# Optimization experiments

Measured on AMD Instinct MI355X. Metric: run time of the kernel, lower is better.

Reference implementation:

```python
import jax, jax.numpy as jnp
import numpy as np

E = 8        # number of sessions (experts)
N = 512      # per-session input width (max units)
P = 512      # n_channels (output width)
F = 100      # max_F time bins
B = 128      # batch of trials
SCALE = 1.0


def setup_inputs() -> dict:
    key = jax.random.key(0)
    kx, ke, k1, k2, k3, k4 = jax.random.split(key, 6)
    x = jax.random.normal(kx, (B, F, N), dtype=jnp.float32)
    eid = jax.random.randint(ke, (B,), 0, E, dtype=jnp.int32)
    # Per-session stitcher Linear(N, 2N) and projector Linear(2N, P), stacked.
    s1 = 1.0 / np.sqrt(N)
    s2 = 1.0 / np.sqrt(2 * N)
    W1 = jax.random.uniform(k1, (E, N, 2 * N), jnp.float32, -s1, s1)
    b1 = jax.random.uniform(k2, (E, 2 * N), jnp.float32, -s1, s1)
    W2 = jax.random.uniform(k3, (E, 2 * N, P), jnp.float32, -s2, s2)
    b2 = jax.random.uniform(k4, (E, P), jnp.float32, -s2, s2)
    return {"x": x, "eid": eid, "W1": W1, "b1": b1, "W2": W2, "b2": b2}


def reference(x, eid, W1, b1, W2, b2):
    # Grouped (per-session) Linear -> Softsign -> Linear, dispatched by eid.
    # Equivalent to the torch loop over unique eids with mask gather/scatter,
    # expressed as a gather of per-sample expert weights + batched matmul.
    w1 = W1[eid]                      # [B, N, 2N]
    stitched = jnp.einsum('bfn,bnh->bfh', x, w1) + b1[eid][:, None, :]
    act = stitched / (1.0 + jnp.abs(stitched))  # Softsign
    act = act * SCALE
    w2 = W2[eid]                      # [B, 2N, P]
    out = jnp.einsum('bfh,bhp->bfp', act, w2) + b2[eid][:, None, :]
    return out                        # [B, F, P]
```

## Files before the change

kernel.cpp:

```cpp
#include <hip/hip_runtime.h>
#include <hip/hip_bf16.h>

#define B_ 128
#define F_ 100
#define N_ 512
#define H_ 1024
#define P_ 512
#define E_ 8
#define BK 64
#define AROWS 112

typedef __attribute__((ext_vector_type(8))) short bf16x8;
typedef __attribute__((ext_vector_type(4))) float f32x4;

#define GLOAD16(g, l) __builtin_amdgcn_global_load_lds(                      \
    (const __attribute__((address_space(1))) void*)(g),                      \
    (__attribute__((address_space(3))) void*)(l), 16, 0, 0)

static __device__ __forceinline__ short f2bf(float f) {
    __hip_bfloat16 h = __float2bfloat16(f);
    short s;
    __builtin_memcpy(&s, &h, sizeof(s));
    return s;
}

__global__ __launch_bounds__(256) void prep(
    const float* __restrict__ x, const float* __restrict__ W1,
    const float* __restrict__ W2, const int* __restrict__ eid,
    short* __restrict__ xbf, short* __restrict__ W1T, short* __restrict__ W2T,
    int2* __restrict__ ttab) {
    __shared__ float tile[64][65];
    __shared__ int scnt[E_], sbase[E_];
    const int bx = blockIdx.x;
    const int t = threadIdx.x;
    if (bx < 3200) {
        const int g = bx * 256 + t;
        const int col = (g & 63) * 8;
        const int row = g >> 6;
        const float* xp = x + (size_t)row * N_ + col;
        const float4 v0 = *(const float4*)(xp);
        const float4 v1 = *(const float4*)(xp + 4);
        union { short s[8]; uint4 u; } o;
        o.s[0] = f2bf(v0.x); o.s[1] = f2bf(v0.y);
        o.s[2] = f2bf(v0.z); o.s[3] = f2bf(v0.w);
        o.s[4] = f2bf(v1.x); o.s[5] = f2bf(v1.y);
        o.s[6] = f2bf(v1.z); o.s[7] = f2bf(v1.w);
        *(uint4*)(xbf + (size_t)row * N_ + col) = o.u;
    } else if (bx < 5248) {
        const float* W; short* WT; int R, C, r0, c0, e;
        if (bx < 4224) {
            const int idx = bx - 3200;
            e = idx >> 7; const int i = idx & 127;
            W = W1; WT = W1T; R = N_; C = H_;
            r0 = (i >> 4) * 64; c0 = (i & 15) * 64;
        } else {
            const int idx = bx - 4224;
            e = idx >> 7; const int i = idx & 127;
            W = W2; WT = W2T; R = H_; C = P_;
            r0 = (i & 15) * 64; c0 = (i >> 4) * 64;
        }
        const float* Wp = W + (size_t)e * R * C;
        short* WTp = WT + (size_t)e * C * R;
        {
            const int c4 = (t & 15) * 4, r = t >> 4;
#pragma unroll
            for (int p = 0; p < 4; p++) {
                const int row = p * 16 + r;
                const float4 v = *(const float4*)(Wp + (size_t)(r0 + row) * C + c0 + c4);
                tile[row][c4 + 0] = v.x; tile[row][c4 + 1] = v.y;
                tile[row][c4 + 2] = v.z; tile[row][c4 + 3] = v.w;
            }
        }
        __syncthreads();
        {
            const int r8 = (t & 7) * 8, cl = t >> 3;
#pragma unroll
            for (int p = 0; p < 2; p++) {
                const int c = p * 32 + cl;
                union { short s[8]; uint4 u; } o;
#pragma unroll
                for (int j = 0; j < 8; j++) o.s[j] = f2bf(tile[r8 + j][c]);
                *(uint4*)(&WTp[(size_t)(c0 + c) * R + r0 + r8]) = o.u;
            }
        }
    } else {
        if (t < E_) scnt[t] = 0;
        __syncthreads();
        int my_e = 0;
        if (t < B_) { my_e = eid[t]; atomicAdd(&scnt[my_e], 1); }
        __syncthreads();
        if (t == 0) {
            int s = 0;
            for (int i = 0; i < E_; i++) { sbase[i] = s; s += scnt[i]; }
        }
        __syncthreads();
        if (t < B_) {
            const int pos = atomicAdd(&sbase[my_e], 1);
            ttab[pos] = make_int2(t, my_e);
        }
    }
}

template <int KDIM, int BN_, bool FIRST>
__global__ __launch_bounds__(256, 2) void gemm_kernel(
    const short* __restrict__ A,
    const short* __restrict__ WT,
    const float* __restrict__ bias,
    const int2* __restrict__ ttab,
    short* __restrict__ actout,
    float* __restrict__ out)
{
    constexpr int NCOLS = FIRST ? H_ : P_;
    constexpr int NI = BN_ / 32;
    constexpr int STAGE1 = (AROWS + BN_) * BK;
    constexpr int EPI_SH = 4 * 4096;
    constexpr int SBUF_SH = (2 * STAGE1 > EPI_SH) ? 2 * STAGE1 : EPI_SH;
    __shared__ short sbuf[SBUF_SH];
    const int slot = (blockIdx.x & 7) * 16 + (blockIdx.x >> 3);
    const int2 te = ttab[slot];
    const int trial = te.x, e = te.y;
    const int n0 = blockIdx.y * BN_;
    const int t = threadIdx.x;
    const int lane = t & 63, w = t >> 6;
    const int wm = (w >> 1) * 64, wn = (w & 1) * (BN_ / 2);
    const int l15 = lane & 15, quad = lane >> 4;
    const int lr = lane >> 3;
    const int lc = (((lane & 7) ^ lr) * 8);

    f32x4 acc[4][NI];
#pragma unroll
    for (int mi = 0; mi < 4; mi++)
#pragma unroll
        for (int ni = 0; ni < NI; ni++)
            acc[mi][ni] = (f32x4)(0.0f);

    float bv[NI];
#pragma unroll
    for (int ni = 0; ni < NI; ni++)
        bv[ni] = bias[(size_t)e * NCOLS + n0 + wn + ni * 16 + l15];

    const short* Ap = A + (size_t)trial * F_ * KDIM;
    const short* Bp = WT + ((size_t)e * NCOLS + n0) * KDIM;

    auto stage = [&](int k0, short* sb) {
        short* sA = sb;
        short* sB = sb + AROWS * BK;
#pragma unroll
        for (int i = 0; i < 4; i++) {
            const int rb = w * 32 + i * 8;
            if (rb < AROWS)
                GLOAD16(Ap + (size_t)(rb + lr) * KDIM + k0 + lc, &sA[rb * BK]);
        }
#pragma unroll
        for (int i = 0; i < NI; i++) {
            const int rb = w * (BN_ / 4) + i * 8;
            GLOAD16(Bp + (size_t)(rb + lr) * KDIM + k0 + lc, &sB[rb * BK]);
        }
    };

    auto compute = [&](const short* sb) {
        const short* sA = sb;
        const short* sB = sb + AROWS * BK;
#pragma unroll
        for (int ks = 0; ks < 2; ks++) {
            const int sw = (((ks * 4 + quad) ^ (l15 & 7)) * 8);
            bf16x8 af, bfr[NI];
#pragma unroll
            for (int ni = 0; ni < NI; ni++)
                bfr[ni] = *(const bf16x8*)(&sB[(wn + ni * 16 + l15) * BK + sw]);
#pragma unroll
            for (int mi = 0; mi < 4; mi++) {
                if (wm + mi * 16 < F_) {
                    af = *(const bf16x8*)(&sA[(wm + mi * 16 + l15) * BK + sw]);
#pragma unroll
                    for (int ni = 0; ni < NI; ni++)
                        acc[mi][ni] = __builtin_amdgcn_mfma_f32_16x16x32_bf16(af, bfr[ni], acc[mi][ni], 0, 0, 0);
                }
            }
        }
    };

    auto wait_prev_and_bar = [&]() {
        if (w < 3) asm volatile("s_waitcnt vmcnt(8)" ::: "memory");
        else       asm volatile("s_waitcnt vmcnt(6)" ::: "memory");
        __builtin_amdgcn_s_barrier();
        __builtin_amdgcn_sched_barrier(0);
    };
    auto bar = [&]() {
        __builtin_amdgcn_sched_barrier(0);
        __builtin_amdgcn_s_barrier();
        __builtin_amdgcn_sched_barrier(0);
    };

    short* b0 = sbuf;
    short* b1 = sbuf + STAGE1;

    stage(0, b0);
    for (int k0 = 0; k0 < KDIM - 2 * BK; k0 += 2 * BK) {
        stage(k0 + BK, b1);
        wait_prev_and_bar();
        compute(b0);
        bar();
        stage(k0 + 2 * BK, b0);
        wait_prev_and_bar();
        compute(b1);
        bar();
    }
    stage(KDIM - BK, b1);
    wait_prev_and_bar();
    compute(b0);
    bar();
    asm volatile("s_waitcnt vmcnt(0)" ::: "memory");
    __builtin_amdgcn_s_barrier();
    __builtin_amdgcn_sched_barrier(0);
    compute(b1);
    bar();

    if constexpr (FIRST) {
        short* sW = sbuf + w * 4096;
#pragma unroll
        for (int mi = 0; mi < 4; mi++) {
#pragma unroll
            for (int ni = 0; ni < 4; ni++) {
                const int cl = ni * 16 + l15;
#pragma unroll
                for (int r = 0; r < 4; r++) {
                    const int rl = mi * 16 + quad * 4 + r;
                    float v = acc[mi][ni][r] + bv[ni];
                    v = v / (1.0f + fabsf(v));
                    sW[rl * 64 + (((cl >> 3) ^ (rl & 7)) * 8) + (cl & 7)] = f2bf(v);
                }
            }
        }
#pragma unroll
        for (int i = 0; i < 8; i++) {
            const int rl = i * 8 + lr;
            const int c = lane & 7;
            const bf16x8 v = *(const bf16x8*)(&sW[rl * 64 + ((c ^ lr) * 8)]);
            const int grow = wm + rl;
            if (grow < F_)
                *(bf16x8*)(&actout[((size_t)trial * F_ + grow) * H_ + n0 + wn + c * 8]) = v;
        }
    } else {
        float* fW = (float*)(sbuf) + w * 2048;
#pragma unroll
        for (int pass = 0; pass < NI; pass += 2) {
#pragma unroll
            for (int mi = 0; mi < 4; mi++) {
#pragma unroll
                for (int nj = 0; nj < 2; nj++) {
                    const int cl = nj * 16 + l15;
#pragma unroll
                    for (int r = 0; r < 4; r++) {
                        const int rl = mi * 16 + quad * 4 + r;
                        fW[rl * 32 + (((cl >> 2) ^ (rl & 7)) * 4) + (cl & 3)] =
                            acc[mi][pass + nj][r] + bv[pass + nj];
                    }
                }
            }
#pragma unroll
            for (int i = 0; i < 8; i++) {
                const int rl = i * 8 + lr;
                const int c = lane & 7;
                const float4 v = *(const float4*)(&fW[rl * 32 + ((c ^ lr) * 4)]);
                const int grow = wm + rl;
                if (grow < F_)
                    *(float4*)(&out[((size_t)trial * F_ + grow) * P_ + n0 + wn + pass * 16 + c * 4]) = v;
            }
        }
    }
}

extern "C" void kernel_launch(void* const* d_in, const int* in_sizes, int n_in,
                              void* d_out, int out_size, void* d_ws, size_t ws_size,
                              hipStream_t stream) {
    const float* x  = (const float*)d_in[0];
    const int* eid  = (const int*)d_in[1];
    const float* W1 = (const float*)d_in[2];
    const float* b1 = (const float*)d_in[3];
    const float* W2 = (const float*)d_in[4];
    const float* b2 = (const float*)d_in[5];
    float* out = (float*)d_out;

    char* ws = (char*)d_ws;
    short* W1T = (short*)(ws);
    short* W2T = (short*)(ws + (size_t)(8u << 20));
    short* act = (short*)(ws + (size_t)(16u << 20));
    short* xbf = (short*)(ws + (size_t)(43u << 20));
    int2* ttab = (int2*)(ws + (size_t)(57u << 20));

    prep<<<dim3(5249), 256, 0, stream>>>(x, W1, W2, eid, xbf, W1T, W2T, ttab);
    gemm_kernel<N_, 128, true><<<dim3(B_, H_ / 128), 256, 0, stream>>>(xbf, W1T, b1, ttab, act, nullptr);
    gemm_kernel<H_, 128, false><<<dim3(B_, P_ / 128), 256, 0, stream>>>(act, W2T, b2, ttab, nullptr, out);
}
```

Baseline: 151.2 us.

## Load weight fragments directly into registers, stage only activations in LDS

The B (weight) operand is no longer staged through shared memory. Each wave now loads its MFMA B fragments straight from global memory into registers, double-buffered across k-steps, while the A tiles stay in LDS via global_load_lds. This halves LDS use per block, so launch bounds go from 2 to 3 blocks per CU, and it removes the LDS reads for B. The cost is more VGPR pressure and uncoalesced 16-byte global loads per lane. The vmcnt wait counts were retuned for the new load mix, which risks ordering bugs if the counts are wrong.

```diff
diff --git a/kernel.cpp b/kernel.cpp
--- a/kernel.cpp
+++ b/kernel.cpp
@@ -101,8 +101,8 @@
     }
 }
 
-template <int KDIM, int BN_, bool FIRST>
-__global__ __launch_bounds__(256, 2) void gemm_kernel(
+template <int KDIM, bool FIRST>
+__global__ __launch_bounds__(256, 3) void gemm_kernel(
     const short* __restrict__ A,
     const short* __restrict__ WT,
     const float* __restrict__ bias,
@@ -111,18 +111,18 @@
     float* __restrict__ out)
 {
     constexpr int NCOLS = FIRST ? H_ : P_;
-    constexpr int NI = BN_ / 32;
-    constexpr int STAGE1 = (AROWS + BN_) * BK;
+    constexpr int NI = 4;
+    constexpr int ASTAGE = AROWS * BK;
     constexpr int EPI_SH = 4 * 4096;
-    constexpr int SBUF_SH = (2 * STAGE1 > EPI_SH) ? 2 * STAGE1 : EPI_SH;
+    constexpr int SBUF_SH = (2 * ASTAGE > EPI_SH) ? 2 * ASTAGE : EPI_SH;
     __shared__ short sbuf[SBUF_SH];
     const int slot = (blockIdx.x & 7) * 16 + (blockIdx.x >> 3);
     const int2 te = ttab[slot];
     const int trial = te.x, e = te.y;
-    const int n0 = blockIdx.y * BN_;
+    const int n0 = blockIdx.y * 128;
     const int t = threadIdx.x;
     const int lane = t & 63, w = t >> 6;
-    const int wm = (w >> 1) * 64, wn = (w & 1) * (BN_ / 2);
+    const int wm = (w >> 1) * 64, wn = (w & 1) * 64;
     const int l15 = lane & 15, quad = lane >> 4;
     const int lr = lane >> 3;
     const int lc = (((lane & 7) ^ lr) * 8);
@@ -140,49 +140,47 @@
         bv[ni] = bias[(size_t)e * NCOLS + n0 + wn + ni * 16 + l15];
 
     const short* Ap = A + (size_t)trial * F_ * KDIM;
-    const short* Bp = WT + ((size_t)e * NCOLS + n0) * KDIM;
-
-    auto stage = [&](int k0, short* sb) {
-        short* sA = sb;
-        short* sB = sb + AROWS * BK;
+    const short* Bp = WT + ((size_t)e * NCOLS + n0 + wn + l15) * KDIM;
+
+    auto stage = [&](int k0, short* sA) {
 #pragma unroll
         for (int i = 0; i < 4; i++) {
             const int rb = w * 32 + i * 8;
             if (rb < AROWS)
                 GLOAD16(Ap + (size_t)(rb + lr) * KDIM + k0 + lc, &sA[rb * BK]);
         }
-#pragma unroll
-        for (int i = 0; i < NI; i++) {
-            const int rb = w * (BN_ / 4) + i * 8;
-            GLOAD16(Bp + (size_t)(rb + lr) * KDIM + k0 + lc, &sB[rb * BK]);
-        }
-    };
-
-    auto compute = [&](const short* sb) {
-        const short* sA = sb;
-        const short* sB = sb + AROWS * BK;
+    };
+
+    auto loadB = [&](int k0, bf16x8 (&br)[2][NI]) {
+#pragma unroll
+        for (int ks = 0; ks < 2; ks++)
+#pragma unroll
+            for (int ni = 0; ni < NI; ni++)
+                br[ks][ni] = *(const bf16x8*)(
+                    Bp + (size_t)(ni * 16) * KDIM + k0 + ks * 32 + quad * 8);
+    };
+
+    auto compute = [&](const short* sA, const bf16x8 (&br)[2][NI]) {
 #pragma unroll
         for (int ks = 0; ks < 2; ks++) {
             const int sw = (((ks * 4 + quad) ^ (l15 & 7)) * 8);
-            bf16x8 af, bfr[NI];
-#pragma unroll
-            for (int ni = 0; ni < NI; ni++)
-                bfr[ni] = *(const bf16x8*)(&sB[(wn + ni * 16 + l15) * BK + sw]);
+            bf16x8 af;
 #pragma unroll
             for (int mi = 0; mi < 4; mi++) {
                 if (wm + mi * 16 < F_) {
                     af = *(const bf16x8*)(&sA[(wm + mi * 16 + l15) * BK + sw]);
 #pragma unroll
                     for (int ni = 0; ni < NI; ni++)
-                        acc[mi][ni] = __builtin_amdgcn_mfma_f32_16x16x32_bf16(af, bfr[ni], acc[mi][ni], 0, 0, 0);
+                        acc[mi][ni] = __builtin_amdgcn_mfma_f32_16x16x32_bf16(af, br[ks][ni], acc[mi][ni], 0, 0, 0);
                 }
             }
         }
     };
 
-    auto wait_prev_and_bar = [&]() {
-        if (w < 3) asm volatile("s_waitcnt vmcnt(8)" ::: "memory");
-        else       asm volatile("s_waitcnt vmcnt(6)" ::: "memory");
+    auto wait_bar = [&](bool last) {
+        if (last)       asm volatile("s_waitcnt vmcnt(8)" ::: "memory");
+        else if (w < 3) asm volatile("s_waitcnt vmcnt(12)" ::: "memory");
+        else            asm volatile("s_waitcnt vmcnt(10)" ::: "memory");
         __builtin_amdgcn_s_barrier();
         __builtin_amdgcn_sched_barrier(0);
     };
@@ -192,29 +190,30 @@
         __builtin_amdgcn_sched_barrier(0);
     };
 
-    short* b0 = sbuf;
-    short* b1 = sbuf + STAGE1;
-
-    stage(0, b0);
-    for (int k0 = 0; k0 < KDIM - 2 * BK; k0 += 2 * BK) {
-        stage(k0 + BK, b1);
-        wait_prev_and_bar();
-        compute(b0);
+    short* a0 = sbuf;
+    short* a1 = sbuf + ASTAGE;
+    bf16x8 brA[2][NI], brB[2][NI];
+
+    stage(0, a0);
+    loadB(0, brA);
+    __builtin_amdgcn_sched_barrier(0);
+    for (int k0 = 0; k0 < KDIM; k0 += 2 * BK) {
+        stage(k0 + BK, a1);
+        __builtin_amdgcn_sched_barrier(0);
+        wait_bar(false);
+        compute(a0, brA);
+        loadB(k0 + BK, brB);
         bar();
-        stage(k0 + 2 * BK, b0);
-        wait_prev_and_bar();
-        compute(b1);
+        const bool more = (k0 + 2 * BK < KDIM);
+        if (more) {
+            stage(k0 + 2 * BK, a0);
+            __builtin_amdgcn_sched_barrier(0);
+        }
+        wait_bar(!more);
+        compute(a1, brB);
+        if (more) loadB(k0 + 2 * BK, brA);
         bar();
     }
-    stage(KDIM - BK, b1);
-    wait_prev_and_bar();
-    compute(b0);
-    bar();
-    asm volatile("s_waitcnt vmcnt(0)" ::: "memory");
-    __builtin_amdgcn_s_barrier();
-    __builtin_amdgcn_sched_barrier(0);
-    compute(b1);
-    bar();
 
     if constexpr (FIRST) {
         short* sW = sbuf + w * 4096;
@@ -290,6 +289,6 @@
     int2* ttab = (int2*)(ws + (size_t)(57u << 20));
 
     prep<<<dim3(5249), 256, 0, stream>>>(x, W1, W2, eid, xbf, W1T, W2T, ttab);
-    gemm_kernel<N_, 128, true><<<dim3(B_, H_ / 128), 256, 0, stream>>>(xbf, W1T, b1, ttab, act, nullptr);
-    gemm_kernel<H_, 128, false><<<dim3(B_, P_ / 128), 256, 0, stream>>>(act, W2T, b2, ttab, nullptr, out);
-}
+    gemm_kernel<N_, true><<<dim3(B_, H_ / 128), 256, 0, stream>>>(xbf, W1T, b1, ttab, act, nullptr);
+    gemm_kernel<H_, false><<<dim3(B_, P_ / 128), 256, 0, stream>>>(act, W2T, b2, ttab, nullptr, out);
+}
```

After: 193.5 us. +27.9%, slower.

## Split first GEMM into dedicated wide-tile kernel with 256-column blocks

Applied to the files above, without the earlier changes.

Replaces the templated first-layer GEMM with a dedicated kernel that computes 256 output columns per block instead of 128, halving the grid and reusing each loaded A tile across twice as many columns. The new kernel uses a simple single-buffered load-sync-compute loop rather than the double-buffered pipeline, and writes the softsign epilogue in two passes. The goal is less redundant reading of the activation input. The cost is higher register use (acc of 4x8 tiles), lost load/compute overlap, and fewer blocks.

```diff
diff --git a/kernel.cpp b/kernel.cpp
--- a/kernel.cpp
+++ b/kernel.cpp
@@ -101,16 +101,116 @@
     }
 }
 
-template <int KDIM, int BN_, bool FIRST>
-__global__ __launch_bounds__(256, 2) void gemm_kernel(
+__global__ __launch_bounds__(256, 2) void gemm1_wide(
     const short* __restrict__ A,
     const short* __restrict__ WT,
     const float* __restrict__ bias,
     const int2* __restrict__ ttab,
-    short* __restrict__ actout,
+    short* __restrict__ actout)
+{
+    constexpr int KDIM = N_;
+    constexpr int NI = 8;
+    __shared__ short sbuf[(AROWS + 256) * BK];
+    short* sA = sbuf;
+    short* sB = sbuf + AROWS * BK;
+    const int slot = (blockIdx.x & 7) * 16 + (blockIdx.x >> 3);
+    const int2 te = ttab[slot];
+    const int trial = te.x, e = te.y;
+    const int n0 = blockIdx.y * 256;
+    const int t = threadIdx.x;
+    const int lane = t & 63, w = t >> 6;
+    const int wm = (w >> 1) * 64, wn = (w & 1) * 128;
+    const int l15 = lane & 15, quad = lane >> 4;
+    const int lr = lane >> 3;
+    const int lc = (((lane & 7) ^ lr) * 8);
+
+    f32x4 acc[4][NI];
+#pragma unroll
+    for (int mi = 0; mi < 4; mi++)
+#pragma unroll
+        for (int ni = 0; ni < NI; ni++)
+            acc[mi][ni] = (f32x4)(0.0f);
+
+    float bv[NI];
+#pragma unroll
+    for (int ni = 0; ni < NI; ni++)
+        bv[ni] = bias[(size_t)e * H_ + n0 + wn + ni * 16 + l15];
+
+    const short* Ap = A + (size_t)trial * F_ * KDIM;
+    const short* Bp = WT + ((size_t)e * H_ + n0) * KDIM;
+
+    for (int k0 = 0; k0 < KDIM; k0 += BK) {
+#pragma unroll
+        for (int i = 0; i < 4; i++) {
+            const int rb = w * 32 + i * 8;
+            if (rb < AROWS)
+                GLOAD16(Ap + (size_t)(rb + lr) * KDIM + k0 + lc, &sA[rb * BK]);
+        }
+#pragma unroll
+        for (int i = 0; i < 8; i++) {
+            const int rb = w * 64 + i * 8;
+            GLOAD16(Bp + (size_t)(rb + lr) * KDIM + k0 + lc, &sB[rb * BK]);
+        }
+        __syncthreads();
+#pragma unroll
+        for (int ks = 0; ks < 2; ks++) {
+            const int sw = (((ks * 4 + quad) ^ (l15 & 7)) * 8);
+            bf16x8 af, bfr[NI];
+#pragma unroll
+            for (int ni = 0; ni < NI; ni++)
+                bfr[ni] = *(const bf16x8*)(&sB[(wn + ni * 16 + l15) * BK + sw]);
+#pragma unroll
+            for (int mi = 0; mi < 4; mi++) {
+                if (wm + mi * 16 < F_) {
+                    af = *(const bf16x8*)(&sA[(wm + mi * 16 + l15) * BK + sw]);
+#pragma unroll
+                    for (int ni = 0; ni < NI; ni++)
+                        acc[mi][ni] = __builtin_amdgcn_mfma_f32_16x16x32_bf16(af, bfr[ni], acc[mi][ni], 0, 0, 0);
+                }
+            }
+        }
+        __syncthreads();
+    }
+
+    short* sW = sbuf + w * 4096;
+#pragma unroll
+    for (int pass = 0; pass < 2; pass++) {
+#pragma unroll
+        for (int mi = 0; mi < 4; mi++) {
+#pragma unroll
+            for (int nj = 0; nj < 4; nj++) {
+                const int ni = pass * 4 + nj;
+                const int cl = nj * 16 + l15;
+#pragma unroll
+                for (int r = 0; r < 4; r++) {
+                    const int rl = mi * 16 + quad * 4 + r;
+                    float v = acc[mi][ni][r] + bv[ni];
+                    v = v / (1.0f + fabsf(v));
+                    sW[rl * 64 + (((cl >> 3) ^ (rl & 7)) * 8) + (cl & 7)] = f2bf(v);
+                }
+            }
+        }
+#pragma unroll
+        for (int i = 0; i < 8; i++) {
+            const int rl = i * 8 + lr;
+            const int c = lane & 7;
+            const bf16x8 v = *(const bf16x8*)(&sW[rl * 64 + ((c ^ lr) * 8)]);
+            const int grow = wm + rl;
+            if (grow < F_)
+                *(bf16x8*)(&actout[((size_t)trial * F_ + grow) * H_ + n0 + wn + pass * 64 + c * 8]) = v;
+        }
+    }
+}
+
+template <int KDIM, int BN_>
+__global__ __launch_bounds__(256, 2) void gemm2_kernel(
+    const short* __restrict__ A,
+    const short* __restrict__ WT,
+    const float* __restrict__ bias,
+    const int2* __restrict__ ttab,
     float* __restrict__ out)
 {
-    constexpr int NCOLS = FIRST ? H_ : P_;
+    constexpr int NCOLS = P_;
     constexpr int NI = BN_ / 32;
     constexpr int STAGE1 = (AROWS + BN_) * BK;
     constexpr int EPI_SH = 4 * 4096;
@@ -216,19 +316,19 @@
     compute(b1);
     bar();
 
-    if constexpr (FIRST) {
-        short* sW = sbuf + w * 4096;
+    float* fW = (float*)(sbuf) + w * 2048;
+#pragma unroll
+    for (int pass = 0; pass < NI; pass += 2) {
 #pragma unroll
         for (int mi = 0; mi < 4; mi++) {
 #pragma unroll
-            for (int ni = 0; ni < 4; ni++) {
-                const int cl = ni * 16 + l15;
+            for (int nj = 0; nj < 2; nj++) {
+                const int cl = nj * 16 + l15;
 #pragma unroll
                 for (int r = 0; r < 4; r++) {
                     const int rl = mi * 16 + quad * 4 + r;
-                    float v = acc[mi][ni][r] + bv[ni];
-                    v = v / (1.0f + fabsf(v));
-                    sW[rl * 64 + (((cl >> 3) ^ (rl & 7)) * 8) + (cl & 7)] = f2bf(v);
+                    fW[rl * 32 + (((cl >> 2) ^ (rl & 7)) * 4) + (cl & 3)] =
+                        acc[mi][pass + nj][r] + bv[pass + nj];
                 }
             }
         }
@@ -236,37 +336,10 @@
         for (int i = 0; i < 8; i++) {
             const int rl = i * 8 + lr;
             const int c = lane & 7;
-            const bf16x8 v = *(const bf16x8*)(&sW[rl * 64 + ((c ^ lr) * 8)]);
+            const float4 v = *(const float4*)(&fW[rl * 32 + ((c ^ lr) * 4)]);
             const int grow = wm + rl;
             if (grow < F_)
-                *(bf16x8*)(&actout[((size_t)trial * F_ + grow) * H_ + n0 + wn + c * 8]) = v;
-        }
-    } else {
-        float* fW = (float*)(sbuf) + w * 2048;
-#pragma unroll
-        for (int pass = 0; pass < NI; pass += 2) {
-#pragma unroll
-            for (int mi = 0; mi < 4; mi++) {
-#pragma unroll
-                for (int nj = 0; nj < 2; nj++) {
-                    const int cl = nj * 16 + l15;
-#pragma unroll
-                    for (int r = 0; r < 4; r++) {
-                        const int rl = mi * 16 + quad * 4 + r;
-                        fW[rl * 32 + (((cl >> 2) ^ (rl & 7)) * 4) + (cl & 3)] =
-                            acc[mi][pass + nj][r] + bv[pass + nj];
-                    }
-                }
-            }
-#pragma unroll
-            for (int i = 0; i < 8; i++) {
-                const int rl = i * 8 + lr;
-                const int c = lane & 7;
-                const float4 v = *(const float4*)(&fW[rl * 32 + ((c ^ lr) * 4)]);
-                const int grow = wm + rl;
-                if (grow < F_)
-                    *(float4*)(&out[((size_t)trial * F_ + grow) * P_ + n0 + wn + pass * 16 + c * 4]) = v;
-            }
+                *(float4*)(&out[((size_t)trial * F_ + grow) * P_ + n0 + wn + pass * 16 + c * 4]) = v;
         }
     }
 }
@@ -290,6 +363,6 @@
     int2* ttab = (int2*)(ws + (size_t)(57u << 20));
 
     prep<<<dim3(5249), 256, 0, stream>>>(x, W1, W2, eid, xbf, W1T, W2T, ttab);
-    gemm_kernel<N_, 128, true><<<dim3(B_, H_ / 128), 256, 0, stream>>>(xbf, W1T, b1, ttab, act, nullptr);
-    gemm_kernel<H_, 128, false><<<dim3(B_, P_ / 128), 256, 0, stream>>>(act, W2T, b2, ttab, nullptr, out);
-}
+    gemm1_wide<<<dim3(B_, H_ / 256), 256, 0, stream>>>(xbf, W1T, b1, ttab, act);
+    gemm2_kernel<H_, 128><<<dim3(B_, P_ / 128), 256, 0, stream>>>(act, W2T, b2, ttab, out);
+}
```

Result: no change. 150.6 us, median of 2 (-0.4%).
